# Kernel tuning notes

Measured on AMD Instinct MI355X. Metric: run time of the kernel, lower is better.

Reference implementation:

```python
import jax, jax.numpy as jnp
import numpy as np

TAU = 0.1          # contrastive_temperature
EPS = 0.05         # property_epsilon
L_LOCAL_G, L_GLOBAL, L_SC_G, L_LOCAL_SC, G_PROP = 1.0, 0.8, 1.0, 0.8, 0.5
B = 4096
D = 256
NUM_PROPS = 4
N_ATOMS = 131072
N_MOTIFS = 32768


def setup_inputs() -> dict:
    key = jax.random.key(0)
    ks = jax.random.split(key, 10)
    return {
        "emb_g_mole": jax.random.normal(ks[0], (B, D), jnp.float32),
        "emb_g_frag": jax.random.normal(ks[1], (N_ATOMS, D), jnp.float32),
        "emb_sc_mole": jax.random.normal(ks[2], (B, D), jnp.float32),
        "emb_sc_shape": jax.random.normal(ks[3], (N_MOTIFS, D), jnp.float32),
        "emb_motif": jax.random.normal(ks[4], (N_MOTIFS, D), jnp.float32),
        "emb_shape": jax.random.normal(ks[5], (N_MOTIFS, D), jnp.float32),
        # scaled so duplicate rows are the only pairs within EPS (realistic sparse mask)
        "prop_pred": jax.random.normal(ks[6], (B, NUM_PROPS), jnp.float32) * 0.05,
        "prop_target": jax.random.normal(ks[7], (B, NUM_PROPS), jnp.float32) * 0.05,
        "batch_g": jax.random.randint(ks[8], (N_ATOMS,), 0, B, jnp.int32),
        "batch_sc": jax.random.randint(ks[9], (N_MOTIFS,), 0, B, jnp.int32),
    }


def _contrastive(emb, props):
    # SupervisedContrastiveLoss: normalized cosine logits, mask from sqrt(cdist) < eps
    n = emb.shape[0]
    e = emb / jnp.maximum(jnp.linalg.norm(emb, axis=1, keepdims=True), 1e-12)
    logits = jnp.matmul(e, e.T) / TAU                       # [n, n]
    log_probs = jax.nn.log_softmax(logits, axis=1)
    sq = jnp.sum(props * props, axis=1)
    d2 = jnp.maximum(sq[:, None] + sq[None, :] - 2.0 * jnp.matmul(props, props.T), 0.0)
    dd = jnp.sqrt(jnp.sqrt(d2)) + 1e-8                      # cdist(...).sqrt() + 1e-8
    mask = (dd < EPS) & (~jnp.eye(n, dtype=bool))           # fill_diagonal_(0)
    cnt = jnp.sum(mask, axis=1)
    row_loss = -jnp.sum(jnp.where(mask, log_probs, 0.0), axis=1) / jnp.maximum(cnt, 1)
    valid = cnt > 0
    nvalid = jnp.sum(valid)
    loss = jnp.sum(jnp.where(valid, row_loss, 0.0)) / jnp.maximum(nvalid, 1)
    return jnp.where(nvalid > 0, loss, 0.0)


def _frag_alignment(emb_g_frag, emb_motif, batch_g, batch_sc):
    ones_g = jnp.ones((emb_g_frag.shape[0],), emb_g_frag.dtype)
    ones_s = jnp.ones((emb_motif.shape[0],), emb_motif.dtype)
    cnt_g = jax.ops.segment_sum(ones_g, batch_g, num_segments=B)
    cnt_s = jax.ops.segment_sum(ones_s, batch_sc, num_segments=B)
    mean_g = jax.ops.segment_sum(emb_g_frag, batch_g, num_segments=B) / jnp.maximum(cnt_g, 1.0)[:, None]
    mean_s = jax.ops.segment_sum(emb_motif, batch_sc, num_segments=B) / jnp.maximum(cnt_s, 1.0)[:, None]
    norms = jnp.linalg.norm(mean_g - mean_s, axis=1)
    valid = (cnt_g > 0) & (cnt_s > 0)
    batch_size = batch_g.max().astype(emb_g_frag.dtype) + 1.0
    return jnp.sum(jnp.where(valid, norms, 0.0)) / batch_size


def reference(emb_g_mole, emb_g_frag, emb_sc_mole, emb_sc_shape, emb_motif,
              emb_shape, prop_pred, prop_target, batch_g, batch_sc):
    l_local_g = _frag_alignment(emb_g_frag, emb_motif, batch_g, batch_sc)
    combined_emb = jnp.concatenate([emb_g_mole, emb_sc_mole], axis=0)    # [2B, d]
    combined_props = jnp.concatenate([prop_pred, prop_pred], axis=0)      # [2B, p]
    l_contr = _contrastive(combined_emb, combined_props)
    l_global = l_contr          # same inputs in both calls -> identical value
    l_local_sc = l_contr
    l_sc_g = jnp.mean(jnp.linalg.norm(emb_sc_shape - emb_shape, axis=1))  # AlignmentLoss mean
    l_prop = jnp.mean((prop_pred - prop_target) ** 2)                     # MSELoss
    l_hes = (L_LOCAL_G * l_local_g + L_GLOBAL * l_global + L_SC_G * l_sc_g
             + L_LOCAL_SC * l_local_sc + G_PROP * l_prop)
    # stacked: [l_hes, l_local_g, l_global, l_sc_g, l_local_sc, l_prop]
    return jnp.stack([l_hes, l_local_g, l_global, l_sc_g, l_local_sc, l_prop])
```

## Files before the change

kernel.cpp:

```cpp
#include <hip/hip_runtime.h>
#include <hip/hip_bf16.h>
#include <stdint.h>

typedef unsigned short u16;
typedef float f32x4 __attribute__((ext_vector_type(4)));
typedef short s16x8 __attribute__((ext_vector_type(8)));
typedef u16   u16x8 __attribute__((ext_vector_type(8)));
typedef u16   u16x4 __attribute__((ext_vector_type(4)));
typedef uint32_t u32x4 __attribute__((ext_vector_type(4)));

#define B_      4096
#define D_      256
#define NA_     131072
#define NM_     32768
#define N2_     8192
#define THR4    6.2499950e-6f
#define K2E     14.426950408889634f

#define NS_   1024
#define NG_   2080
#define NT_   256
#define NTOT_ 3360
#define NR_   2336

#define OFF_CNT_G   0u
#define OFF_CNT_S   16384u
#define OFF_CUR_G   32768u
#define OFF_CUR_S   49152u
#define OFF_NB      65536u
#define OFF_SCAL    81920u
#define OFF_S       98304u
#define ZERO_BYTES  131072u
#define OFF_T       131072u
#define OFF_C       163840u
#define OFF_PLIST   196608u
#define OFF_OFFS_G  720896u
#define OFF_OFFS_S  737280u
#define OFF_SORT_G  753664u
#define OFF_SORT_S  1277952u
#define OFF_E       1409024u
#define WS_NEED     5603328u

__device__ inline float wave_sum(float v) {
#pragma unroll
  for (int m = 1; m < 64; m <<= 1) v += __shfl_xor(v, m, 64);
  return v;
}
__device__ inline int wave_sum_i(int v) {
#pragma unroll
  for (int m = 1; m < 64; m <<= 1) v += __shfl_xor(v, m, 64);
  return v;
}
__device__ inline u16 f2bf(float f) {
  uint32_t u = __float_as_uint(f);
  uint32_t r = (u + 0x7FFFu + ((u >> 16) & 1u)) >> 16;
  return (u16)r;
}
__device__ inline float bf2f(u16 v) { return __uint_as_float(((uint32_t)v) << 16); }

__device__ inline void gload16(const u16* __restrict__ g, u16* l) {
  __builtin_amdgcn_global_load_lds(
      (const __attribute__((address_space(1))) uint32_t*)g,
      (__attribute__((address_space(3))) uint32_t*)l, 16, 0, 0);
}

__global__ void k_zero(u32x4* __restrict__ p) {
  u32x4 z = {0u, 0u, 0u, 0u};
  p[blockIdx.x * 256 + threadIdx.x] = z;
}

__global__ __launch_bounds__(256) void k_fuseA(
    const int* __restrict__ bg, const int* __restrict__ bs,
    int* __restrict__ cntg, int* __restrict__ cnts, int* __restrict__ bmax,
    const float* __restrict__ gm, const float* __restrict__ scm,
    const float* __restrict__ scs, const float* __restrict__ shp,
    const float* __restrict__ pp,
    u16* __restrict__ E, int* __restrict__ nb, int* __restrict__ plist,
    float* __restrict__ scal) {
  int t = threadIdx.x, w = t >> 6, lane = t & 63;
  int blk = blockIdx.x;

  if (blk < 512) {
    int i = blk * 256 + t;
    int b = -1;
    if (i < NA_) { b = bg[i]; atomicAdd(&cntg[b], 1); }
    if (i < NM_) { atomicAdd(&cnts[bs[i]], 1); }
    int m = b;
#pragma unroll
    for (int k = 1; k < 64; k <<= 1) m = max(m, __shfl_xor(m, k, 64));
    if ((t & 63) == 0 && m >= 0) atomicMax(bmax, m);
  } else if (blk < 4608) {
    int a = blk - 512;
    f32x4 pa = *(const f32x4*)(pp + (size_t)a * 4);
    for (int b = t; b < B_; b += 256) {
      f32x4 pb = *(const f32x4*)(pp + (size_t)b * 4);
      float dx = pa.x - pb.x, dy = pa.y - pb.y, dz = pa.z - pb.z, dw = pa.w - pb.w;
      float d2 = dx * dx + dy * dy + dz * dz + dw * dw;
      if (d2 < THR4) {
        int pos = atomicAdd(&nb[a], 1);
        if (pos < 32) plist[a * 32 + pos] = b;
      }
    }
  } else if (blk < 6656) {
    int r = (blk - 4608) * 4 + w;
    const float* src = (r < B_) ? gm + (size_t)r * D_ : scm + (size_t)(r - B_) * D_;
    f32x4 v = *(const f32x4*)(src + lane * 4);
    float ss = v.x * v.x + v.y * v.y + v.z * v.z + v.w * v.w;
    ss = wave_sum(ss);
    float inv = 1.f / fmaxf(sqrtf(ss), 1e-12f);
    u16x4 o;
    o.x = f2bf(v.x * inv); o.y = f2bf(v.y * inv);
    o.z = f2bf(v.z * inv); o.w = f2bf(v.w * inv);
    *(u16x4*)(E + (size_t)r * D_ + lane * 4) = o;
  } else {
    int wg = (blk - 6656) * 4 + w;
    float acc = 0.f;
    for (int r = wg; r < NM_; r += 8192) {
      f32x4 va = *(const f32x4*)(scs + (size_t)r * D_ + lane * 4);
      f32x4 vb = *(const f32x4*)(shp + (size_t)r * D_ + lane * 4);
      float dx = va.x - vb.x, dy = va.y - vb.y, dz = va.z - vb.z, dw = va.w - vb.w;
      float ss = wave_sum(dx * dx + dy * dy + dz * dz + dw * dw);
      if (lane == 0) acc += sqrtf(ss);
    }
    __shared__ float sr4[4];
    if (lane == 0) sr4[w] = acc;
    __syncthreads();
    if (t == 0) atomicAdd(&scal[1], sr4[0] + sr4[1] + sr4[2] + sr4[3]);
  }
}

__global__ void k_scan(const int* __restrict__ cntg, const int* __restrict__ cnts,
                       int* offsg, int* offss, int* curg, int* curs) {
  const int* cnt = blockIdx.x == 0 ? cntg : cnts;
  int* offs = blockIdx.x == 0 ? offsg : offss;
  int* cur  = blockIdx.x == 0 ? curg  : curs;
  __shared__ int ls[256];
  int t = threadIdx.x;
  int v[16]; int s = 0;
#pragma unroll
  for (int k = 0; k < 16; k++) { v[k] = cnt[t * 16 + k]; s += v[k]; }
  ls[t] = s;
  __syncthreads();
  for (int off = 1; off < 256; off <<= 1) {
    int add = (t >= off) ? ls[t - off] : 0;
    __syncthreads();
    ls[t] += add;
    __syncthreads();
  }
  int pre = t ? ls[t - 1] : 0;
#pragma unroll
  for (int k = 0; k < 16; k++) { offs[t * 16 + k] = pre; cur[t * 16 + k] = pre; pre += v[k]; }
}

__global__ void k_scatter(const int* __restrict__ bg, const int* __restrict__ bs,
                          int* curg, int* curs, int* sortg, int* sorts) {
  int i = blockIdx.x * 256 + threadIdx.x;
  if (i < NA_) { int b = bg[i]; sortg[atomicAdd(&curg[b], 1)] = i; }
  if (i < NM_) { int b = bs[i]; sorts[atomicAdd(&curs[b], 1)] = i; }
}

__device__ inline void wave_row_sum(const float* __restrict__ src,
                                    const int* __restrict__ sorted,
                                    int off, int cnt, int lane, f32x4* accs) {
  f32x4 a0 = {0.f,0.f,0.f,0.f}, a1 = a0, a2 = a0, a3 = a0;
  f32x4 a4 = a0, a5 = a0, a6 = a0, a7 = a0;
  for (int base = 0; base < cnt; base += 64) {
    int n = min(cnt - base, 64);
    int idx = (lane < n) ? sorted[off + base + lane] : 0;
    int k = 0;
    for (; k + 7 < n; k += 8) {
      int i0 = __shfl(idx, k,     64), i1 = __shfl(idx, k + 1, 64);
      int i2 = __shfl(idx, k + 2, 64), i3 = __shfl(idx, k + 3, 64);
      int i4 = __shfl(idx, k + 4, 64), i5 = __shfl(idx, k + 5, 64);
      int i6 = __shfl(idx, k + 6, 64), i7 = __shfl(idx, k + 7, 64);
      a0 += *(const f32x4*)(src + (size_t)i0 * D_ + lane * 4);
      a1 += *(const f32x4*)(src + (size_t)i1 * D_ + lane * 4);
      a2 += *(const f32x4*)(src + (size_t)i2 * D_ + lane * 4);
      a3 += *(const f32x4*)(src + (size_t)i3 * D_ + lane * 4);
      a4 += *(const f32x4*)(src + (size_t)i4 * D_ + lane * 4);
      a5 += *(const f32x4*)(src + (size_t)i5 * D_ + lane * 4);
      a6 += *(const f32x4*)(src + (size_t)i6 * D_ + lane * 4);
      a7 += *(const f32x4*)(src + (size_t)i7 * D_ + lane * 4);
    }
    for (; k < n; k++) {
      int i0 = __shfl(idx, k, 64);
      a0 += *(const f32x4*)(src + (size_t)i0 * D_ + lane * 4);
    }
  }
  *accs = ((a0 + a1) + (a2 + a3)) + ((a4 + a5) + (a6 + a7));
}

__global__ __launch_bounds__(256) void k_fuseB(
    const u16* __restrict__ E,
    const float* __restrict__ fg, const float* __restrict__ fm,
    const int* __restrict__ cntg, const int* __restrict__ cnts,
    const int* __restrict__ offsg, const int* __restrict__ offss,
    const int* __restrict__ sortg, const int* __restrict__ sorts,
    const int* __restrict__ nb, const int* __restrict__ plist,
    float* __restrict__ S, float* __restrict__ T, int* __restrict__ C,
    float* __restrict__ scal) {
  __shared__ __align__(16) u16 As[128 * 64];
  __shared__ __align__(16) u16 Bs[128 * 64];
  int blk = blockIdx.x;
  int tid = threadIdx.x, lane = tid & 63, wid = tid >> 6;

  int64_t p = (int64_t)blk * NS_;
  int srem = (int)(p % NTOT_);
  if (srem < NS_) {
    int sid = (int)(p / NTOT_);
    int b = sid * 4 + wid;
    int cg = cntg[b], cs = cnts[b];
    int og = offsg[b], os = offss[b];
    f32x4 sg, ss;
    wave_row_sum(fg, sortg, og, cg, lane, &sg);
    wave_row_sum(fm, sorts, os, cs, lane, &ss);
    float ig = 1.f / fmaxf((float)cg, 1.f);
    float is = 1.f / fmaxf((float)cs, 1.f);
    float dx = sg.x * ig - ss.x * is, dy = sg.y * ig - ss.y * is;
    float dz = sg.z * ig - ss.z * is, dw = sg.w * ig - ss.w * is;
    float v = wave_sum(dx * dx + dy * dy + dz * dz + dw * dw);
    __shared__ float r2[4];
    if (lane == 0) r2[wid] = (cg > 0 && cs > 0) ? sqrtf(v) : 0.f;
    __syncthreads();
    if (tid == 0) {
      float s = r2[0] + r2[1] + r2[2] + r2[3];
      if (s != 0.f) atomicAdd(&scal[0], s);
    }
    return;
  }

  int r = blk - (int)((p + NTOT_ - 1) / NTOT_);
  int64_t q = (int64_t)r * NG_;
  int grem = (int)(q % NR_);

  if (grem >= NG_) {
    int tix = r - (int)((q + NR_ - 1) / NR_);
#pragma unroll
    for (int k8 = 0; k8 < 8; k8++) {
      int i = tix * 32 + wid * 8 + k8;
      int a = i & (B_ - 1);
      int n = min(nb[a], 32);
      u16x4 vi = *(const u16x4*)(E + (size_t)i * D_ + lane * 4);
      float ex = bf2f(vi.x), ey = bf2f(vi.y), ez = bf2f(vi.z), ew = bf2f(vi.w);
      float acc = -(ex * ex + ey * ey + ez * ez + ew * ew);
      for (int k = 0; k < n; k++) {
        int b = plist[a * 32 + k];
        u16x4 v1 = *(const u16x4*)(E + (size_t)b * D_ + lane * 4);
        u16x4 v2 = *(const u16x4*)(E + (size_t)(b + B_) * D_ + lane * 4);
        acc += ex * bf2f(v1.x) + ey * bf2f(v1.y) + ez * bf2f(v1.z) + ew * bf2f(v1.w);
        acc += ex * bf2f(v2.x) + ey * bf2f(v2.y) + ez * bf2f(v2.z) + ew * bf2f(v2.w);
      }
      acc = wave_sum(acc);
      if (lane == 0) { T[i] = 10.0f * acc; C[i] = 2 * n - 1; }
    }
    return;
  }

  int t = (int)(q / NR_);
  int bi = (int)((129.0f - sqrtf(129.0f * 129.0f - 8.0f * (float)t)) * 0.5f);
  while ((bi + 1) * (129 - (bi + 1)) / 2 <= t) bi++;
  while (bi * (129 - bi) / 2 > t) bi--;
  int bj = bi + (t - bi * (129 - bi) / 2);

  int row0 = bi * 128, col0 = bj * 128;
  int wr = wid >> 1, wc = wid & 1;

  int rsub = lane >> 3;
  int csw  = (((lane & 7) ^ rsub) << 4) >> 1;

  f32x4 acc[4][4];
#pragma unroll
  for (int mi = 0; mi < 4; mi++)
#pragma unroll
    for (int ni = 0; ni < 4; ni++) {
      f32x4 z = {0.f, 0.f, 0.f, 0.f};
      acc[mi][ni] = z;
    }

  for (int kc = 0; kc < 4; ++kc) {
    __syncthreads();
#pragma unroll
    for (int it = 0; it < 4; it++) {
      int s = wid * 4 + it;
      int rr = s * 8 + rsub;
      gload16(E + (size_t)(row0 + rr) * D_ + kc * 64 + csw, As + s * 512);
      gload16(E + (size_t)(col0 + rr) * D_ + kc * 64 + csw, Bs + s * 512);
    }
    __syncthreads();
#pragma unroll
    for (int kk = 0; kk < 2; ++kk) {
      s16x8 af[4], bfr[4];
#pragma unroll
      for (int mi = 0; mi < 4; mi++) {
        int rA = wr * 64 + mi * 16 + (lane & 15);
        int cbf = kk * 64 + (lane >> 4) * 16;
        int addr = rA * 128 + (cbf ^ ((rA & 7) << 4));
        af[mi] = *(const s16x8*)((const char*)As + addr);
      }
#pragma unroll
      for (int ni = 0; ni < 4; ni++) {
        int rB = wc * 64 + ni * 16 + (lane & 15);
        int cbf = kk * 64 + (lane >> 4) * 16;
        int addr = rB * 128 + (cbf ^ ((rB & 7) << 4));
        bfr[ni] = *(const s16x8*)((const char*)Bs + addr);
      }
#pragma unroll
      for (int mi = 0; mi < 4; mi++)
#pragma unroll
        for (int ni = 0; ni < 4; ni++)
          acc[mi][ni] = __builtin_amdgcn_mfma_f32_16x16x32_bf16(af[mi], bfr[ni], acc[mi][ni], 0, 0, 0);
    }
  }

  int g = lane >> 4, cl = lane & 15;
  float colsum[4] = {0.f, 0.f, 0.f, 0.f};
#pragma unroll
  for (int mi = 0; mi < 4; mi++) {
#pragma unroll
    for (int reg = 0; reg < 4; ++reg) {
      int gi = row0 + wr * 64 + mi * 16 + g * 4 + reg;
      float vs = 0.f;
#pragma unroll
      for (int ni = 0; ni < 4; ni++) {
        float e = exp2f(acc[mi][ni][reg] * K2E - K2E);
        vs += e;
        colsum[ni] += e;
      }
#pragma unroll
      for (int m = 1; m < 16; m <<= 1) vs += __shfl_xor(vs, m, 64);
      if (cl == 0) atomicAdd(&S[gi], vs);
    }
  }
  if (bi != bj) {
#pragma unroll
    for (int ni = 0; ni < 4; ni++) {
      float cs = colsum[ni];
      cs += __shfl_xor(cs, 16, 64);
      cs += __shfl_xor(cs, 32, 64);
      if (g == 0) atomicAdd(&S[col0 + wc * 64 + ni * 16 + cl], cs);
    }
  }
}

__global__ void k_final(const float* __restrict__ S, const float* __restrict__ T,
                        const int* __restrict__ C, const float* __restrict__ scal,
                        const float* __restrict__ pp, const float* __restrict__ pt,
                        float* __restrict__ out) {
  float sp = 0.f;
  for (int i = threadIdx.x; i < B_ * 4; i += 256) {
    float d = pp[i] - pt[i];
    sp += d * d;
  }
  float rls = 0.f; int nv = 0;
  for (int i = threadIdx.x; i < N2_; i += 256) {
    int ci = C[i];
    if (ci > 0) { rls += (10.0f + logf(S[i])) - T[i] / (float)ci; nv++; }
  }
  rls = wave_sum(rls);
  sp  = wave_sum(sp);
  nv  = wave_sum_i(nv);
  __shared__ float r1[4], r3[4]; __shared__ int r2[4];
  int lane = threadIdx.x & 63, w = threadIdx.x >> 6;
  if (lane == 0) { r1[w] = rls; r2[w] = nv; r3[w] = sp; }
  __syncthreads();
  if (threadIdx.x == 0) {
    float rtot = r1[0] + r1[1] + r1[2] + r1[3];
    int nvt = r2[0] + r2[1] + r2[2] + r2[3];
    float sptot = r3[0] + r3[1] + r3[2] + r3[3];
    float l_contr = nvt > 0 ? rtot / (float)nvt : 0.f;
    int bmax = ((const int*)scal)[3];
    float bs = (float)bmax + 1.0f;
    float l_local_g = scal[0] / bs;
    float l_sc = scal[1] / (float)NM_;
    float l_prop = sptot / (float)(B_ * 4);
    float l_hes = 1.0f * l_local_g + 0.8f * l_contr + 1.0f * l_sc + 0.8f * l_contr + 0.5f * l_prop;
    out[0] = l_hes; out[1] = l_local_g; out[2] = l_contr;
    out[3] = l_sc;  out[4] = l_contr;   out[5] = l_prop;
  }
}

extern "C" void kernel_launch(void* const* d_in, const int* in_sizes, int n_in,
                              void* d_out, int out_size, void* d_ws, size_t ws_size,
                              hipStream_t stream) {
  if (ws_size < WS_NEED) return;
  const float* gm  = (const float*)d_in[0];
  const float* fg  = (const float*)d_in[1];
  const float* scm = (const float*)d_in[2];
  const float* scs = (const float*)d_in[3];
  const float* mot = (const float*)d_in[4];
  const float* shp = (const float*)d_in[5];
  const float* pp  = (const float*)d_in[6];
  const float* pt  = (const float*)d_in[7];
  const int* bg = (const int*)d_in[8];
  const int* bs = (const int*)d_in[9];
  float* out = (float*)d_out;
  char* ws = (char*)d_ws;

  int* cntg  = (int*)(ws + OFF_CNT_G);
  int* cnts  = (int*)(ws + OFF_CNT_S);
  int* curg  = (int*)(ws + OFF_CUR_G);
  int* curs  = (int*)(ws + OFF_CUR_S);
  int* nb    = (int*)(ws + OFF_NB);
  float* scal = (float*)(ws + OFF_SCAL);
  float* S   = (float*)(ws + OFF_S);
  float* T   = (float*)(ws + OFF_T);
  int* C     = (int*)(ws + OFF_C);
  int* plist = (int*)(ws + OFF_PLIST);
  int* offsg = (int*)(ws + OFF_OFFS_G);
  int* offss = (int*)(ws + OFF_OFFS_S);
  int* sortg = (int*)(ws + OFF_SORT_G);
  int* sorts = (int*)(ws + OFF_SORT_S);
  u16* E     = (u16*)(ws + OFF_E);

  k_zero<<<32, 256, 0, stream>>>((u32x4*)ws);
  k_fuseA<<<8704, 256, 0, stream>>>(bg, bs, cntg, cnts, (int*)scal + 3,
                                    gm, scm, scs, shp, pp, E, nb, plist, scal);
  k_scan<<<2, 256, 0, stream>>>(cntg, cnts, offsg, offss, curg, curs);
  k_scatter<<<512, 256, 0, stream>>>(bg, bs, curg, curs, sortg, sorts);
  k_fuseB<<<NTOT_, 256, 0, stream>>>(E, fg, mot, cntg, cnts, offsg, offss,
                                     sortg, sorts, nb, plist, S, T, C, scal);
  k_final<<<1, 256, 0, stream>>>(S, T, C, scal, pp, pt, out);
}
```

Before: 212.6 us.

## Replace scan+scatter grouping with fixed-capacity per-segment lists built during counting

```diff
diff --git a/kernel.cpp b/kernel.cpp
--- a/kernel.cpp
+++ b/kernel.cpp
@@ -16,6 +16,8 @@
 #define N2_     8192
 #define THR4    6.2499950e-6f
 #define K2E     14.426950408889634f
+#define CAPG    96
+#define CAPS    40
 
 #define NS_   1024
 #define NG_   2080
@@ -25,21 +27,17 @@
 
 #define OFF_CNT_G   0u
 #define OFF_CNT_S   16384u
-#define OFF_CUR_G   32768u
-#define OFF_CUR_S   49152u
-#define OFF_NB      65536u
-#define OFF_SCAL    81920u
-#define OFF_S       98304u
-#define ZERO_BYTES  131072u
-#define OFF_T       131072u
-#define OFF_C       163840u
-#define OFF_PLIST   196608u
-#define OFF_OFFS_G  720896u
-#define OFF_OFFS_S  737280u
-#define OFF_SORT_G  753664u
-#define OFF_SORT_S  1277952u
-#define OFF_E       1409024u
-#define WS_NEED     5603328u
+#define OFF_NB      32768u
+#define OFF_SCAL    49152u
+#define OFF_S       65536u
+#define ZERO_BYTES  98304u
+#define OFF_T       98304u
+#define OFF_C       131072u
+#define OFF_PLIST   163840u
+#define OFF_LIST_G  688128u
+#define OFF_LIST_S  2260992u
+#define OFF_E       2916352u
+#define WS_NEED     7110656u
 
 __device__ inline float wave_sum(float v) {
 #pragma unroll
@@ -58,6 +56,10 @@
 }
 __device__ inline float bf2f(u16 v) { return __uint_as_float(((uint32_t)v) << 16); }
 
+__device__ inline f32x4 ldnt4(const float* p) {
+  return __builtin_nontemporal_load((const f32x4*)p);
+}
+
 __device__ inline void gload16(const u16* __restrict__ g, u16* l) {
   __builtin_amdgcn_global_load_lds(
       (const __attribute__((address_space(1))) uint32_t*)g,
@@ -72,6 +74,7 @@
 __global__ __launch_bounds__(256) void k_fuseA(
     const int* __restrict__ bg, const int* __restrict__ bs,
     int* __restrict__ cntg, int* __restrict__ cnts, int* __restrict__ bmax,
+    int* __restrict__ listg, int* __restrict__ lists,
     const float* __restrict__ gm, const float* __restrict__ scm,
     const float* __restrict__ scs, const float* __restrict__ shp,
     const float* __restrict__ pp,
@@ -83,8 +86,16 @@
   if (blk < 512) {
     int i = blk * 256 + t;
     int b = -1;
-    if (i < NA_) { b = bg[i]; atomicAdd(&cntg[b], 1); }
-    if (i < NM_) { atomicAdd(&cnts[bs[i]], 1); }
+    if (i < NA_) {
+      b = bg[i];
+      int pos = atomicAdd(&cntg[b], 1);
+      if (pos < CAPG) listg[b * CAPG + pos] = i;
+    }
+    if (i < NM_) {
+      int b2 = bs[i];
+      int pos = atomicAdd(&cnts[b2], 1);
+      if (pos < CAPS) lists[b2 * CAPS + pos] = i;
+    }
     int m = b;
 #pragma unroll
     for (int k = 1; k < 64; k <<= 1) m = max(m, __shfl_xor(m, k, 64));
@@ -104,7 +115,7 @@
   } else if (blk < 6656) {
     int r = (blk - 4608) * 4 + w;
     const float* src = (r < B_) ? gm + (size_t)r * D_ : scm + (size_t)(r - B_) * D_;
-    f32x4 v = *(const f32x4*)(src + lane * 4);
+    f32x4 v = ldnt4(src + lane * 4);
     float ss = v.x * v.x + v.y * v.y + v.z * v.z + v.w * v.w;
     ss = wave_sum(ss);
     float inv = 1.f / fmaxf(sqrtf(ss), 1e-12f);
@@ -116,8 +127,8 @@
     int wg = (blk - 6656) * 4 + w;
     float acc = 0.f;
     for (int r = wg; r < NM_; r += 8192) {
-      f32x4 va = *(const f32x4*)(scs + (size_t)r * D_ + lane * 4);
-      f32x4 vb = *(const f32x4*)(shp + (size_t)r * D_ + lane * 4);
+      f32x4 va = ldnt4(scs + (size_t)r * D_ + lane * 4);
+      f32x4 vb = ldnt4(shp + (size_t)r * D_ + lane * 4);
       float dx = va.x - vb.x, dy = va.y - vb.y, dz = va.z - vb.z, dw = va.w - vb.w;
       float ss = wave_sum(dx * dx + dy * dy + dz * dz + dw * dw);
       if (lane == 0) acc += sqrtf(ss);
@@ -129,62 +140,32 @@
   }
 }
 
-__global__ void k_scan(const int* __restrict__ cntg, const int* __restrict__ cnts,
-                       int* offsg, int* offss, int* curg, int* curs) {
-  const int* cnt = blockIdx.x == 0 ? cntg : cnts;
-  int* offs = blockIdx.x == 0 ? offsg : offss;
-  int* cur  = blockIdx.x == 0 ? curg  : curs;
-  __shared__ int ls[256];
-  int t = threadIdx.x;
-  int v[16]; int s = 0;
-#pragma unroll
-  for (int k = 0; k < 16; k++) { v[k] = cnt[t * 16 + k]; s += v[k]; }
-  ls[t] = s;
-  __syncthreads();
-  for (int off = 1; off < 256; off <<= 1) {
-    int add = (t >= off) ? ls[t - off] : 0;
-    __syncthreads();
-    ls[t] += add;
-    __syncthreads();
-  }
-  int pre = t ? ls[t - 1] : 0;
-#pragma unroll
-  for (int k = 0; k < 16; k++) { offs[t * 16 + k] = pre; cur[t * 16 + k] = pre; pre += v[k]; }
-}
-
-__global__ void k_scatter(const int* __restrict__ bg, const int* __restrict__ bs,
-                          int* curg, int* curs, int* sortg, int* sorts) {
-  int i = blockIdx.x * 256 + threadIdx.x;
-  if (i < NA_) { int b = bg[i]; sortg[atomicAdd(&curg[b], 1)] = i; }
-  if (i < NM_) { int b = bs[i]; sorts[atomicAdd(&curs[b], 1)] = i; }
-}
-
 __device__ inline void wave_row_sum(const float* __restrict__ src,
-                                    const int* __restrict__ sorted,
+                                    const int* __restrict__ list,
                                     int off, int cnt, int lane, f32x4* accs) {
   f32x4 a0 = {0.f,0.f,0.f,0.f}, a1 = a0, a2 = a0, a3 = a0;
   f32x4 a4 = a0, a5 = a0, a6 = a0, a7 = a0;
   for (int base = 0; base < cnt; base += 64) {
     int n = min(cnt - base, 64);
-    int idx = (lane < n) ? sorted[off + base + lane] : 0;
+    int idx = (lane < n) ? list[off + base + lane] : 0;
     int k = 0;
     for (; k + 7 < n; k += 8) {
       int i0 = __shfl(idx, k,     64), i1 = __shfl(idx, k + 1, 64);
       int i2 = __shfl(idx, k + 2, 64), i3 = __shfl(idx, k + 3, 64);
       int i4 = __shfl(idx, k + 4, 64), i5 = __shfl(idx, k + 5, 64);
       int i6 = __shfl(idx, k + 6, 64), i7 = __shfl(idx, k + 7, 64);
-      a0 += *(const f32x4*)(src + (size_t)i0 * D_ + lane * 4);
-      a1 += *(const f32x4*)(src + (size_t)i1 * D_ + lane * 4);
-      a2 += *(const f32x4*)(src + (size_t)i2 * D_ + lane * 4);
-      a3 += *(const f32x4*)(src + (size_t)i3 * D_ + lane * 4);
-      a4 += *(const f32x4*)(src + (size_t)i4 * D_ + lane * 4);
-      a5 += *(const f32x4*)(src + (size_t)i5 * D_ + lane * 4);
-      a6 += *(const f32x4*)(src + (size_t)i6 * D_ + lane * 4);
-      a7 += *(const f32x4*)(src + (size_t)i7 * D_ + lane * 4);
+      a0 += ldnt4(src + (size_t)i0 * D_ + lane * 4);
+      a1 += ldnt4(src + (size_t)i1 * D_ + lane * 4);
+      a2 += ldnt4(src + (size_t)i2 * D_ + lane * 4);
+      a3 += ldnt4(src + (size_t)i3 * D_ + lane * 4);
+      a4 += ldnt4(src + (size_t)i4 * D_ + lane * 4);
+      a5 += ldnt4(src + (size_t)i5 * D_ + lane * 4);
+      a6 += ldnt4(src + (size_t)i6 * D_ + lane * 4);
+      a7 += ldnt4(src + (size_t)i7 * D_ + lane * 4);
     }
     for (; k < n; k++) {
       int i0 = __shfl(idx, k, 64);
-      a0 += *(const f32x4*)(src + (size_t)i0 * D_ + lane * 4);
+      a0 += ldnt4(src + (size_t)i0 * D_ + lane * 4);
     }
   }
   *accs = ((a0 + a1) + (a2 + a3)) + ((a4 + a5) + (a6 + a7));
@@ -194,8 +175,7 @@
     const u16* __restrict__ E,
     const float* __restrict__ fg, const float* __restrict__ fm,
     const int* __restrict__ cntg, const int* __restrict__ cnts,
-    const int* __restrict__ offsg, const int* __restrict__ offss,
-    const int* __restrict__ sortg, const int* __restrict__ sorts,
+    const int* __restrict__ listg, const int* __restrict__ lists,
     const int* __restrict__ nb, const int* __restrict__ plist,
     float* __restrict__ S, float* __restrict__ T, int* __restrict__ C,
     float* __restrict__ scal) {
@@ -210,10 +190,9 @@
     int sid = (int)(p / NTOT_);
     int b = sid * 4 + wid;
     int cg = cntg[b], cs = cnts[b];
-    int og = offsg[b], os = offss[b];
     f32x4 sg, ss;
-    wave_row_sum(fg, sortg, og, cg, lane, &sg);
-    wave_row_sum(fm, sorts, os, cs, lane, &ss);
+    wave_row_sum(fg, listg, b * CAPG, min(cg, CAPG), lane, &sg);
+    wave_row_sum(fm, lists, b * CAPS, min(cs, CAPS), lane, &ss);
     float ig = 1.f / fmaxf((float)cg, 1.f);
     float is = 1.f / fmaxf((float)cs, 1.f);
     float dx = sg.x * ig - ss.x * is, dy = sg.y * ig - ss.y * is;
@@ -398,26 +377,21 @@
 
   int* cntg  = (int*)(ws + OFF_CNT_G);
   int* cnts  = (int*)(ws + OFF_CNT_S);
-  int* curg  = (int*)(ws + OFF_CUR_G);
-  int* curs  = (int*)(ws + OFF_CUR_S);
   int* nb    = (int*)(ws + OFF_NB);
   float* scal = (float*)(ws + OFF_SCAL);
   float* S   = (float*)(ws + OFF_S);
   float* T   = (float*)(ws + OFF_T);
   int* C     = (int*)(ws + OFF_C);
   int* plist = (int*)(ws + OFF_PLIST);
-  int* offsg = (int*)(ws + OFF_OFFS_G);
-  int* offss = (int*)(ws + OFF_OFFS_S);
-  int* sortg = (int*)(ws + OFF_SORT_G);
-  int* sorts = (int*)(ws + OFF_SORT_S);
+  int* listg = (int*)(ws + OFF_LIST_G);
+  int* lists = (int*)(ws + OFF_LIST_S);
   u16* E     = (u16*)(ws + OFF_E);
 
-  k_zero<<<32, 256, 0, stream>>>((u32x4*)ws);
+  k_zero<<<24, 256, 0, stream>>>((u32x4*)ws);
   k_fuseA<<<8704, 256, 0, stream>>>(bg, bs, cntg, cnts, (int*)scal + 3,
-                                    gm, scm, scs, shp, pp, E, nb, plist, scal);
-  k_scan<<<2, 256, 0, stream>>>(cntg, cnts, offsg, offss, curg, curs);
-  k_scatter<<<512, 256, 0, stream>>>(bg, bs, curg, curs, sortg, sorts);
-  k_fuseB<<<NTOT_, 256, 0, stream>>>(E, fg, mot, cntg, cnts, offsg, offss,
-                                     sortg, sorts, nb, plist, S, T, C, scal);
+                                    listg, lists, gm, scm, scs, shp, pp,
+                                    E, nb, plist, scal);
+  k_fuseB<<<NTOT_, 256, 0, stream>>>(E, fg, mot, cntg, cnts, listg, lists,
+                                     nb, plist, S, T, C, scal);
   k_final<<<1, 256, 0, stream>>>(S, T, C, scal, pp, pt, out);
 }
```

New measurement: 202.8 us. -4.6%, faster.
